# Performance work log

Hardware: AMD Instinct MI355X
Metric: run time of the kernel (lower is better)

The kernel has to match this reference:

```python
import jax, jax.numpy as jnp
import numpy as np

N_NODES = 100000
N_EDGES = 1600000
IN_FEATS = 128
OUT_FEATS = 128
LN_EPS = 1e-5


def setup_inputs() -> dict:
    key = jax.random.key(0)
    k1, k2, k3, k4, k5 = jax.random.split(key, 5)
    h = jax.random.normal(k1, (N_NODES, IN_FEATS), dtype=jnp.float32)
    # nn.Linear(2*in_feats, out_feats): weight [out, 2*in], bias [out]
    stdv = 1.0 / np.sqrt(2 * IN_FEATS)
    W = jax.random.uniform(k2, (OUT_FEATS, 2 * IN_FEATS), dtype=jnp.float32, minval=-stdv, maxval=stdv)
    b = jax.random.uniform(k3, (OUT_FEATS,), dtype=jnp.float32, minval=-stdv, maxval=stdv)
    gamma = jnp.ones((OUT_FEATS,), dtype=jnp.float32)
    beta = jnp.zeros((OUT_FEATS,), dtype=jnp.float32)
    src = jax.random.randint(k4, (N_EDGES,), 0, N_NODES, dtype=jnp.int32)
    dst = jax.random.randint(k5, (N_EDGES,), 0, N_NODES, dtype=jnp.int32)
    return {"h": h, "W": W, "b": b, "gamma": gamma, "beta": beta, "src": src, "dst": dst}


def reference(h, W, b, gamma, beta, src, dst):
    n = h.shape[0]
    ones = jnp.ones(src.shape[0], dtype=h.dtype)
    deg = jax.ops.segment_sum(ones, dst, num_segments=n)          # in-degrees [N]
    norm = jnp.where(deg > 0, 1.0 / deg, 0.0)[:, None]            # inf -> 0
    ah = jax.ops.segment_sum(h[src], dst, num_segments=n)         # copy_src + sum: [N, D]
    cat = jnp.concatenate([h, ah * norm], axis=1)                 # [N, 2D]
    y = cat @ W.T + b                                             # linear -> [N, OUT]
    mu = jnp.mean(y, axis=-1, keepdims=True)
    var = jnp.mean((y - mu) ** 2, axis=-1, keepdims=True)
    y = (y - mu) * jax.lax.rsqrt(var + LN_EPS) * gamma + beta     # LayerNorm
    return jax.nn.relu(y)
```

## Files before the change

### kernel.cpp

```cpp
#include <hip/hip_runtime.h>
#include <hip/hip_bf16.h>

#define LN_EPS 1e-5f

#define NW 4096
#define CHUNK_CAP 96

#define CAP2 1280

typedef __attribute__((ext_vector_type(8))) short short8;
typedef __attribute__((ext_vector_type(4))) float f32x4;
typedef __attribute__((ext_vector_type(2))) float f32x2;
typedef __attribute__((ext_vector_type(4))) int int4v;
typedef __attribute__((ext_vector_type(4))) unsigned int uint4v;

#if defined(__has_builtin)
# if __has_builtin(__builtin_amdgcn_cvt_pk_f32_fp8)
#  define HAS_HW_FP8 1
# endif
#endif
#ifndef HAS_HW_FP8
# define HAS_HW_FP8 0
#endif

__device__ __forceinline__ float b2f(unsigned short u) {
    union { unsigned int i; float f; } x; x.i = ((unsigned int)u) << 16; return x.f;
}
__device__ __forceinline__ unsigned short f2b(float f) {
    unsigned int u = __float_as_uint(f);
    unsigned int r = (u + 0x7FFFu + ((u >> 16) & 1u)) >> 16;
    return (unsigned short)r;
}
__device__ __forceinline__ float loadf(const void* p, long long i, int flag) {
    return flag ? ((const float*)p)[i] : b2f(((const unsigned short*)p)[i]);
}

__device__ __forceinline__ unsigned char f2fp8(float x) {
    float ax = fabsf(x);
    unsigned char s = (unsigned char)((__float_as_uint(x) >> 24) & 0x80);
    if (ax >= 448.f) return s | 0x7E;
    if (ax < 0.015625f) {
        int m = (int)(ax * 512.f + 0.5f);
        return s | (unsigned char)m;
    }
    unsigned u = __float_as_uint(ax);
    int e = (int)((u >> 23) & 0xFF) - 127;
    unsigned m = u & 0x7FFFFF;
    unsigned mr = (m + 0x7FFFF + ((m >> 20) & 1)) >> 20;
    unsigned val = (unsigned)((e + 7) << 3) + mr;
    if (val > 0x7E) val = 0x7E;
    return s | (unsigned char)val;
}
__device__ __forceinline__ float fp8d(unsigned v) {
    unsigned s = (v & 0x80) << 24;
    unsigned e = (v >> 3) & 0xF;
    unsigned m = v & 7;
    if (e == 0) {
        float f = (float)m * 0.001953125f;
        return __uint_as_float(s | __float_as_uint(f));
    }
    return __uint_as_float(s | ((e + 120) << 23) | (m << 20));
}
__device__ __forceinline__ void dec16(uint4 u, float* acc) {
#if HAS_HW_FP8
    f32x2 p;
    p = __builtin_amdgcn_cvt_pk_f32_fp8((int)u.x, false); acc[0] += p[0];  acc[1] += p[1];
    p = __builtin_amdgcn_cvt_pk_f32_fp8((int)u.x, true);  acc[2] += p[0];  acc[3] += p[1];
    p = __builtin_amdgcn_cvt_pk_f32_fp8((int)u.y, false); acc[4] += p[0];  acc[5] += p[1];
    p = __builtin_amdgcn_cvt_pk_f32_fp8((int)u.y, true);  acc[6] += p[0];  acc[7] += p[1];
    p = __builtin_amdgcn_cvt_pk_f32_fp8((int)u.z, false); acc[8] += p[0];  acc[9] += p[1];
    p = __builtin_amdgcn_cvt_pk_f32_fp8((int)u.z, true);  acc[10] += p[0]; acc[11] += p[1];
    p = __builtin_amdgcn_cvt_pk_f32_fp8((int)u.w, false); acc[12] += p[0]; acc[13] += p[1];
    p = __builtin_amdgcn_cvt_pk_f32_fp8((int)u.w, true);  acc[14] += p[0]; acc[15] += p[1];
#else
    acc[0] += fp8d(u.x & 0xFF); acc[1] += fp8d((u.x >> 8) & 0xFF);
    acc[2] += fp8d((u.x >> 16) & 0xFF); acc[3] += fp8d(u.x >> 24);
    acc[4] += fp8d(u.y & 0xFF); acc[5] += fp8d((u.y >> 8) & 0xFF);
    acc[6] += fp8d((u.y >> 16) & 0xFF); acc[7] += fp8d(u.y >> 24);
    acc[8] += fp8d(u.z & 0xFF); acc[9] += fp8d((u.z >> 8) & 0xFF);
    acc[10] += fp8d((u.z >> 16) & 0xFF); acc[11] += fp8d(u.z >> 24);
    acc[12] += fp8d(u.w & 0xFF); acc[13] += fp8d((u.w >> 8) & 0xFF);
    acc[14] += fp8d((u.w >> 16) & 0xFF); acc[15] += fp8d(u.w >> 24);
#endif
}

__global__ __launch_bounds__(256) void prep_cvt_kernel(
    const void* __restrict__ h, unsigned char* __restrict__ h8,
    int* __restrict__ cnt, int* __restrict__ flag, int n_nodes, int n16) {
    __shared__ int sflag;
    const int tid = threadIdx.x;
    if (tid < 64) {
        const unsigned short* hb = (const unsigned short*)h;
        int bad = 0;
        unsigned short u = hb[2 * tid];        int e = (u >> 7) & 0xFF; bad += (e < 96 || e > 135);
        u = hb[2 * (tid + 64)];                e = (u >> 7) & 0xFF;     bad += (e < 96 || e > 135);
#pragma unroll
        for (int off = 1; off < 64; off <<= 1) bad += __shfl_xor(bad, off);
        if (tid == 0) sflag = (bad > 32) ? 1 : 0;
    }
    __syncthreads();
    const int f = sflag;
    const int idx = blockIdx.x * 256 + tid;
    if (idx < n_nodes) cnt[idx] = 0;
    if (idx == 0) *flag = f;
    if (idx < n16) {
        long long base = (long long)idx * 16;
        union { uint4 v; unsigned char b[16]; } o;
        if (f == 0) {
            const unsigned short* hb = (const unsigned short*)h + base;
#pragma unroll
            for (int j = 0; j < 16; ++j) o.b[j] = f2fp8(b2f(hb[j]));
        } else {
            const float* hf = (const float*)h + base;
#pragma unroll
            for (int j = 0; j < 16; ++j) o.b[j] = f2fp8(hf[j]);
        }
        *(uint4*)(h8 + base) = o.v;
    }
}

__global__ __launch_bounds__(256) void bin_kernel(
    const int* __restrict__ src, const int* __restrict__ dst,
    long long* __restrict__ bins,
    int* __restrict__ wcnt,
    int n_edges, int part_nodes) {
    const int g = blockIdx.x * 4 + (threadIdx.x >> 6);
    const int lane = threadIdx.x & 63;
    const int epw = (n_edges + NW - 1) / NW;
    const int e0 = g * epw;
    const int e1 = min(e0 + epw, n_edges);
    const unsigned long long below = (1ull << lane) - 1ull;
    const int t4 = part_nodes * 4, t2 = part_nodes * 2;

    int cur0 = 0, cur1 = 0, cur2 = 0, cur3 = 0, cur4 = 0, cur5 = 0, cur6 = 0, cur7 = 0;

    for (int e = e0 + lane;; e += 64) {
        const bool valid = (e < e1);
        if (!__ballot(valid)) break;
        int d = 0, s = 0;
        if (valid) {
            d = __builtin_nontemporal_load(&dst[e]);
            s = __builtin_nontemporal_load(&src[e]);
        }
        int p = 0, dd = d;
        if (dd >= t4) { p += 4; dd -= t4; }
        if (dd >= t2) { p += 2; dd -= t2; }
        if (dd >= part_nodes) { p += 1; }

        int myoff = CHUNK_CAP;
#pragma unroll
        for (int pp = 0; pp < 8; ++pp) {
            const unsigned long long m = __ballot(valid && (p == pp));
            const int rank = __popcll(m & below);
            const int n = __popcll(m);
            int c = (pp == 0) ? cur0 : (pp == 1) ? cur1 : (pp == 2) ? cur2 :
                    (pp == 3) ? cur3 : (pp == 4) ? cur4 : (pp == 5) ? cur5 :
                    (pp == 6) ? cur6 : cur7;
            if (valid && (p == pp)) myoff = c + rank;
            c += n;
            if (pp == 0) cur0 = c; else if (pp == 1) cur1 = c;
            else if (pp == 2) cur2 = c; else if (pp == 3) cur3 = c;
            else if (pp == 4) cur4 = c; else if (pp == 5) cur5 = c;
            else if (pp == 6) cur6 = c; else cur7 = c;
        }
        if (valid && myoff < CHUNK_CAP) {
            const long long pr = ((long long)(unsigned)d << 32) | (unsigned)s;
            bins[((long long)g * 8 + p) * CHUNK_CAP + myoff] = pr;
        }
    }
    int myc = cur0;
    myc = (lane == 1) ? cur1 : myc;  myc = (lane == 2) ? cur2 : myc;
    myc = (lane == 3) ? cur3 : myc;  myc = (lane == 4) ? cur4 : myc;
    myc = (lane == 5) ? cur5 : myc;  myc = (lane == 6) ? cur6 : myc;
    myc = (lane == 7) ? cur7 : myc;
    if (lane < 8) wcnt[g * 8 + lane] = min(myc, CHUNK_CAP);
}

__global__ __launch_bounds__(256) void regroup_kernel(
    const long long* __restrict__ bins, const int* __restrict__ wcnt,
    long long* __restrict__ bins2, int* __restrict__ gcur,
    int part_nodes) {
    __shared__ int bcnt[256], gbase_s[256], bcur_s[256];
    const int part = blockIdx.x & 7;
    const int rng  = blockIdx.x >> 3;
    const int wbase = rng * 64;
    const int tid = threadIdx.x;
    const int fb_lo = (part * part_nodes) >> 6;
    bcnt[tid] = 0;
    __syncthreads();
    const int wv = tid >> 6, lane = tid & 63;
    for (int c = wv; c < 64; c += 4) {
        const int w = wbase + c;
        const int n = wcnt[w * 8 + part];
        const long long* cb = bins + ((long long)w * 8 + part) * CHUNK_CAP;
        for (int i = lane; i < n; i += 64) {
            const int d = (int)((unsigned long long)cb[i] >> 32);
            atomicAdd(&bcnt[(d >> 6) - fb_lo], 1);
        }
    }
    __syncthreads();
    {
        const int c = bcnt[tid];
        gbase_s[tid] = (c > 0) ? atomicAdd(&gcur[fb_lo + tid], c) : 0;
        bcur_s[tid] = 0;
    }
    __syncthreads();
    for (int c = wv; c < 64; c += 4) {
        const int w = wbase + c;
        const int n = wcnt[w * 8 + part];
        const long long* cb = bins + ((long long)w * 8 + part) * CHUNK_CAP;
        for (int i = lane; i < n; i += 64) {
            const long long pr = cb[i];
            const int d = (int)((unsigned long long)pr >> 32);
            const int lb = (d >> 6) - fb_lo;
            const int r = atomicAdd(&bcur_s[lb], 1);
            const int pos = gbase_s[lb] + r;
            if (pos < CAP2)
                bins2[(long long)(fb_lo + lb) * CAP2 + pos] = pr;
        }
    }
}

__global__ __launch_bounds__(256) void gather_gemm_ln_kernel(
    const unsigned char* __restrict__ h8,
    const long long* __restrict__ bins2,
    const int* __restrict__ gcur,
    const void* __restrict__ h,
    const void* __restrict__ W,
    const void* __restrict__ bias,
    const void* __restrict__ gamma,
    const void* __restrict__ beta,
    void* __restrict__ out,
    const int* __restrict__ flagp,
    int n_nodes) {

    __shared__ __align__(16) unsigned short Atile[64 * 264];
    __shared__ __align__(16) char pool[CAP2 * 4 * 2 + CAP2];
    __shared__ int ncnt[64], noff[64], ncur[64];
    __shared__ unsigned char perm[64];
    __shared__ float2 mrs[64];

    int* sraw = (int*)pool;
    int* slist = sraw + CAP2;
    unsigned char* draw = (unsigned char*)(slist + CAP2);
    float2* pS = (float2*)pool;

    const int flag = *flagp;
    const int tid = threadIdx.x;
    const int fb = blockIdx.x;
    const int nb0 = fb << 6;

    {
        const int seg = tid & 31;
        const int r0 = tid >> 5;
        if (seg < 16) {
            if (flag == 0) {
                const unsigned short* hb = (const unsigned short*)h;
#pragma unroll
                for (int j = 0; j < 8; ++j) {
                    int row = r0 + j * 8;
                    int node = nb0 + row;
                    if (node >= n_nodes) node = n_nodes - 1;
                    short8 val = __builtin_nontemporal_load(
                        (const short8*)(hb + (long long)node * 128 + seg * 8));
                    *(short8*)&Atile[row * 264 + seg * 8] = val;
                }
            } else {
                const float* hfp = (const float*)h;
#pragma unroll
                for (int j = 0; j < 8; ++j) {
                    int row = r0 + j * 8;
                    int node = nb0 + row;
                    if (node >= n_nodes) node = n_nodes - 1;
                    const float* p = hfp + (long long)node * 128 + seg * 8;
                    f32x4 a = __builtin_nontemporal_load((const f32x4*)p);
                    f32x4 b4 = __builtin_nontemporal_load(((const f32x4*)p) + 1);
                    short8 val;
                    val[0] = (short)f2b(a[0]);  val[1] = (short)f2b(a[1]);
                    val[2] = (short)f2b(a[2]);  val[3] = (short)f2b(a[3]);
                    val[4] = (short)f2b(b4[0]); val[5] = (short)f2b(b4[1]);
                    val[6] = (short)f2b(b4[2]); val[7] = (short)f2b(b4[3]);
                    *(short8*)&Atile[row * 264 + seg * 8] = val;
                }
            }
        }
    }

    if (tid < 64) ncnt[tid] = 0;
    __syncthreads();
    const int T = min(gcur[fb], CAP2);
    const long long* bb = bins2 + (long long)fb * CAP2;
    for (int i = tid; i < T; i += 256) {
        const long long pr = __builtin_nontemporal_load(&bb[i]);
        const int ld = ((int)((unsigned long long)pr >> 32)) & 63;
        sraw[i] = (int)(pr & 0xFFFFFFFFll);
        draw[i] = (unsigned char)ld;
        atomicAdd(&ncnt[ld], 1);
    }
    __syncthreads();
    if (tid < 64) {
        const int mydeg = ncnt[tid];
        int o = 0, rk = 0;
#pragma unroll 1
        for (int j = 0; j < 64; ++j) {
            const int dj = ncnt[j];
            o += (j < tid) ? dj : 0;
            rk += (dj > mydeg) || (dj == mydeg && j < tid);
        }
        noff[tid] = o; ncur[tid] = 0;
        perm[rk] = (unsigned char)tid;
    }
    __syncthreads();
    for (int i = tid; i < T; i += 256) {
        const int ld = draw[i];
        const int r = atomicAdd(&ncur[ld], 1);
        slist[noff[ld] + r] = sraw[i];
    }
    __syncthreads();

    const int wv = tid >> 6, lane = tid & 63, g = lane >> 3, li = lane & 7;
#pragma unroll 1
    for (int pass = 0; pass < 2; ++pass) {
        const int rank = (pass * 8 + g) * 4 + wv;
        const int ld = perm[rank];
        const int node = nb0 + ld;
        const bool nvalid = (node < n_nodes);
        const int deg = nvalid ? ncnt[ld] : 0;
        const int ofs = noff[ld];
        int mn = deg, mx = deg;
        mn = min(mn, __shfl_xor(mn, 8));  mx = max(mx, __shfl_xor(mx, 8));
        mn = min(mn, __shfl_xor(mn, 16)); mx = max(mx, __shfl_xor(mx, 16));
        mn = min(mn, __shfl_xor(mn, 32)); mx = max(mx, __shfl_xor(mx, 32));

        float acc[16];
#pragma unroll
        for (int j = 0; j < 16; ++j) acc[j] = 0.f;

        int e = 0;
        for (; e + 1 < mn; e += 2) {
            const int s0 = slist[ofs + e];
            const int s1 = slist[ofs + e + 1];
            uint4 u0 = *(const uint4*)(h8 + (long long)s0 * 128 + li * 16);
            uint4 u1 = *(const uint4*)(h8 + (long long)s1 * 128 + li * 16);
            dec16(u0, acc);
            dec16(u1, acc);
        }
        for (; e < mx; ++e) {
            const bool v = (e < deg);
            const int s = slist[min(ofs + (v ? e : 0), CAP2 - 1)];
            uint4 u = *(const uint4*)(h8 + (long long)(v ? s : 0) * 128 + li * 16);
            if (!v) { u.x = 0u; u.y = 0u; u.z = 0u; u.w = 0u; }
            dec16(u, acc);
        }

        const float nrm = deg > 0 ? 1.f / (float)deg : 0.f;
        short8 a0, a1;
        a0[0] = (short)f2b(acc[0] * nrm);  a0[1] = (short)f2b(acc[1] * nrm);
        a0[2] = (short)f2b(acc[2] * nrm);  a0[3] = (short)f2b(acc[3] * nrm);
        a0[4] = (short)f2b(acc[4] * nrm);  a0[5] = (short)f2b(acc[5] * nrm);
        a0[6] = (short)f2b(acc[6] * nrm);  a0[7] = (short)f2b(acc[7] * nrm);
        a1[0] = (short)f2b(acc[8] * nrm);  a1[1] = (short)f2b(acc[9] * nrm);
        a1[2] = (short)f2b(acc[10] * nrm); a1[3] = (short)f2b(acc[11] * nrm);
        a1[4] = (short)f2b(acc[12] * nrm); a1[5] = (short)f2b(acc[13] * nrm);
        a1[6] = (short)f2b(acc[14] * nrm); a1[7] = (short)f2b(acc[15] * nrm);
        *(short8*)&Atile[ld * 264 + 128 + li * 16] = a0;
        *(short8*)&Atile[ld * 264 + 128 + li * 16 + 8] = a1;
    }
    __syncthreads();

    const int q = lane >> 4;
    const int c = lane & 15;

    short8 bfrag[8][2];
    if (flag == 0) {
        const unsigned short* Wb = (const unsigned short*)W;
#pragma unroll
        for (int ki = 0; ki < 8; ++ki)
#pragma unroll
            for (int t2 = 0; t2 < 2; ++t2)
                bfrag[ki][t2] = *(const short8*)&Wb[(wv * 32 + t2 * 16 + c) * 256 + ki * 32 + q * 8];
    } else {
        const float* Wf = (const float*)W;
#pragma unroll
        for (int ki = 0; ki < 8; ++ki)
#pragma unroll
            for (int t2 = 0; t2 < 2; ++t2) {
                const float* p = Wf + (wv * 32 + t2 * 16 + c) * 256 + ki * 32 + q * 8;
#pragma unroll
                for (int j = 0; j < 8; ++j) bfrag[ki][t2][j] = (short)f2b(p[j]);
            }
    }

    f32x4 acc2[4][2];
#pragma unroll
    for (int rc = 0; rc < 4; ++rc)
#pragma unroll
        for (int t2 = 0; t2 < 2; ++t2) acc2[rc][t2] = (f32x4){0.f, 0.f, 0.f, 0.f};

#pragma unroll
    for (int ki = 0; ki < 8; ++ki) {
        const int kk = ki * 32 + q * 8;
#pragma unroll
        for (int rc = 0; rc < 4; ++rc) {
            const short8 a = *(const short8*)&Atile[(rc * 16 + c) * 264 + kk];
            acc2[rc][0] = __builtin_amdgcn_mfma_f32_16x16x32_bf16(a, bfrag[ki][0], acc2[rc][0], 0, 0, 0);
            acc2[rc][1] = __builtin_amdgcn_mfma_f32_16x16x32_bf16(a, bfrag[ki][1], acc2[rc][1], 0, 0, 0);
        }
    }

    float bcol[2], gcol[2], ecol[2];
#pragma unroll
    for (int t2 = 0; t2 < 2; ++t2) {
        int col = wv * 32 + t2 * 16 + c;
        bcol[t2] = loadf(bias, col, flag);
        gcol[t2] = loadf(gamma, col, flag);
        ecol[t2] = loadf(beta, col, flag);
    }

#pragma unroll
    for (int rc = 0; rc < 4; ++rc)
#pragma unroll
        for (int r = 0; r < 4; ++r) {
            float v0 = acc2[rc][0][r] + bcol[0];
            float v1 = acc2[rc][1][r] + bcol[1];
            float s = v0 + v1;
            float ss = v0 * v0 + v1 * v1;
            s += __shfl_xor(s, 1);  ss += __shfl_xor(ss, 1);
            s += __shfl_xor(s, 2);  ss += __shfl_xor(ss, 2);
            if ((c & 3) == 0) {
                int row = rc * 16 + q * 4 + r;
                pS[row * 17 + (wv * 4 + (c >> 2))] = make_float2(s, ss);
            }
        }
    __syncthreads();

    if (tid < 64) {
        float s = 0.f, ss = 0.f;
#pragma unroll
        for (int j = 0; j < 16; ++j) {
            float2 p = pS[tid * 17 + j];
            s += p.x; ss += p.y;
        }
        float mean = s * (1.f / 128.f);
        float var = ss * (1.f / 128.f) - mean * mean;
        mrs[tid] = make_float2(mean, rsqrtf(var + LN_EPS));
    }
    __syncthreads();

#pragma unroll
    for (int rc = 0; rc < 4; ++rc)
#pragma unroll
        for (int r = 0; r < 4; ++r) {
            int row = rc * 16 + q * 4 + r;
            int node = nb0 + row;
            if (node < n_nodes) {
                float2 m = mrs[row];
#pragma unroll
                for (int t2 = 0; t2 < 2; ++t2) {
                    float o = (acc2[rc][t2][r] + bcol[t2] - m.x) * m.y * gcol[t2] + ecol[t2];
                    o = o > 0.f ? o : 0.f;
                    long long idx = (long long)node * 128 + wv * 32 + t2 * 16 + c;
                    if (flag) ((float*)out)[idx] = o;
                    else      ((unsigned short*)out)[idx] = f2b(o);
                }
            }
        }
}

extern "C" void kernel_launch(void* const* d_in, const int* in_sizes, int n_in,
                              void* d_out, int out_size, void* d_ws, size_t ws_size,
                              hipStream_t stream) {
    const void* h     = d_in[0];
    const void* W     = d_in[1];
    const void* b     = d_in[2];
    const void* gamma = d_in[3];
    const void* beta  = d_in[4];
    const int* src = (const int*)d_in[5];
    const int* dst = (const int*)d_in[6];

    const int n_nodes = in_sizes[0] / 128;
    const int n_edges = in_sizes[5];
    const int part_nodes = (n_nodes + 7) / 8;
    const int nbuckets = (n_nodes + 63) >> 6;

    unsigned short* reg0 = (unsigned short*)d_ws;
    long long* bins2 = (long long*)(reg0 + (size_t)n_nodes * 128);
    int* gcur   = (int*)(bins2) + (size_t)n_nodes * 64;
    int* flag   = gcur + n_nodes;
    unsigned char* h8 = (unsigned char*)(flag + 64);

    long long* bins = (long long*)reg0;
    int* wcnt = (int*)((char*)reg0 + (size_t)NW * 8 * CHUNK_CAP * 8);

    int n16 = n_nodes * 8;
    int pgrid = (max(n16, n_nodes) + 255) / 256;
    prep_cvt_kernel<<<pgrid, 256, 0, stream>>>(h, h8, gcur, flag, n_nodes, n16);

    bin_kernel<<<NW / 4, 256, 0, stream>>>(src, dst, bins, wcnt, n_edges, part_nodes);

    regroup_kernel<<<512, 256, 0, stream>>>(bins, wcnt, bins2, gcur, part_nodes);

    gather_gemm_ln_kernel<<<nbuckets, 256, 0, stream>>>(h8, bins2, gcur, h, W, b,
                                                        gamma, beta, d_out, flag, n_nodes);
}
```

Measured before the change: 275.6 us.

## Pack edge pairs into 32-bit words, use hardware FP8 encode, unroll gather by four

Edge (dst,src) pairs are packed into one 32-bit word (local dst offset in high bits, 17-bit src) instead of 64-bit pairs. This halves bin and bin2 traffic and removes the shared-memory staging copy in the gather kernel, which now re-reads the packed words. The prep conversion uses vector loads and the hardware fp8 pack instruction, and the neighbor gather loop issues four row loads per iteration for more memory-level parallelism. The LayerNorm partial reduction is also done with more shuffles to shrink shared writes. The 17-bit src field limits node count to 131072 and the local dst field to what fits in 15 bits.

```diff
diff --git a/kernel.cpp b/kernel.cpp
--- a/kernel.cpp
+++ b/kernel.cpp
@@ -7,6 +7,8 @@
 #define CHUNK_CAP 96
 
 #define CAP2 1280
+
+#define S_MASK 0x1FFFFu
 
 typedef __attribute__((ext_vector_type(8))) short short8;
 typedef __attribute__((ext_vector_type(4))) float f32x4;
@@ -18,9 +20,15 @@
 # if __has_builtin(__builtin_amdgcn_cvt_pk_f32_fp8)
 #  define HAS_HW_FP8 1
 # endif
+# if __has_builtin(__builtin_amdgcn_cvt_pk_fp8_f32)
+#  define HAS_HW_FP8E 1
+# endif
 #endif
 #ifndef HAS_HW_FP8
 # define HAS_HW_FP8 0
+#endif
+#ifndef HAS_HW_FP8E
+# define HAS_HW_FP8E 0
 #endif
 
 __device__ __forceinline__ float b2f(unsigned short u) {
@@ -50,6 +58,16 @@
     unsigned val = (unsigned)((e + 7) << 3) + mr;
     if (val > 0x7E) val = 0x7E;
     return s | (unsigned char)val;
+}
+__device__ __forceinline__ unsigned enc4(float a, float b, float c, float d) {
+#if HAS_HW_FP8E
+    int r = __builtin_amdgcn_cvt_pk_fp8_f32(a, b, 0, false);
+    r = __builtin_amdgcn_cvt_pk_fp8_f32(c, d, r, true);
+    return (unsigned)r;
+#else
+    return (unsigned)f2fp8(a) | ((unsigned)f2fp8(b) << 8) |
+           ((unsigned)f2fp8(c) << 16) | ((unsigned)f2fp8(d) << 24);
+#endif
 }
 __device__ __forceinline__ float fp8d(unsigned v) {
     unsigned s = (v & 0x80) << 24;
@@ -105,23 +123,37 @@
     if (idx == 0) *flag = f;
     if (idx < n16) {
         long long base = (long long)idx * 16;
-        union { uint4 v; unsigned char b[16]; } o;
+        uint4 o;
         if (f == 0) {
-            const unsigned short* hb = (const unsigned short*)h + base;
-#pragma unroll
-            for (int j = 0; j < 16; ++j) o.b[j] = f2fp8(b2f(hb[j]));
+            const unsigned short* hp = (const unsigned short*)h + base;
+            short8 v0 = *(const short8*)hp;
+            short8 v1 = *(const short8*)(hp + 8);
+            o.x = enc4(b2f((unsigned short)v0[0]), b2f((unsigned short)v0[1]),
+                       b2f((unsigned short)v0[2]), b2f((unsigned short)v0[3]));
+            o.y = enc4(b2f((unsigned short)v0[4]), b2f((unsigned short)v0[5]),
+                       b2f((unsigned short)v0[6]), b2f((unsigned short)v0[7]));
+            o.z = enc4(b2f((unsigned short)v1[0]), b2f((unsigned short)v1[1]),
+                       b2f((unsigned short)v1[2]), b2f((unsigned short)v1[3]));
+            o.w = enc4(b2f((unsigned short)v1[4]), b2f((unsigned short)v1[5]),
+                       b2f((unsigned short)v1[6]), b2f((unsigned short)v1[7]));
         } else {
             const float* hf = (const float*)h + base;
-#pragma unroll
-            for (int j = 0; j < 16; ++j) o.b[j] = f2fp8(hf[j]);
-        }
-        *(uint4*)(h8 + base) = o.v;
+            f32x4 a = *(const f32x4*)hf;
+            f32x4 b4 = *(const f32x4*)(hf + 4);
+            f32x4 c4 = *(const f32x4*)(hf + 8);
+            f32x4 d4 = *(const f32x4*)(hf + 12);
+            o.x = enc4(a[0], a[1], a[2], a[3]);
+            o.y = enc4(b4[0], b4[1], b4[2], b4[3]);
+            o.z = enc4(c4[0], c4[1], c4[2], c4[3]);
+            o.w = enc4(d4[0], d4[1], d4[2], d4[3]);
+        }
+        *(uint4*)(h8 + base) = o;
     }
 }
 
 __global__ __launch_bounds__(256) void bin_kernel(
     const int* __restrict__ src, const int* __restrict__ dst,
-    long long* __restrict__ bins,
+    unsigned* __restrict__ bins,
     int* __restrict__ wcnt,
     int n_edges, int part_nodes) {
     const int g = blockIdx.x * 4 + (threadIdx.x >> 6);
@@ -145,7 +177,7 @@
         int p = 0, dd = d;
         if (dd >= t4) { p += 4; dd -= t4; }
         if (dd >= t2) { p += 2; dd -= t2; }
-        if (dd >= part_nodes) { p += 1; }
+        if (dd >= part_nodes) { p += 1; dd -= part_nodes; }
 
         int myoff = CHUNK_CAP;
 #pragma unroll
@@ -164,7 +196,7 @@
             else if (pp == 6) cur6 = c; else cur7 = c;
         }
         if (valid && myoff < CHUNK_CAP) {
-            const long long pr = ((long long)(unsigned)d << 32) | (unsigned)s;
+            const unsigned pr = ((unsigned)dd << 17) | (unsigned)s;
             bins[((long long)g * 8 + p) * CHUNK_CAP + myoff] = pr;
         }
     }
@@ -177,25 +209,26 @@
 }
 
 __global__ __launch_bounds__(256) void regroup_kernel(
-    const long long* __restrict__ bins, const int* __restrict__ wcnt,
-    long long* __restrict__ bins2, int* __restrict__ gcur,
+    const unsigned* __restrict__ bins, const int* __restrict__ wcnt,
+    unsigned* __restrict__ bins2, int* __restrict__ gcur,
     int part_nodes) {
     __shared__ int bcnt[256], gbase_s[256], bcur_s[256];
     const int part = blockIdx.x & 7;
     const int rng  = blockIdx.x >> 3;
     const int wbase = rng * 64;
     const int tid = threadIdx.x;
-    const int fb_lo = (part * part_nodes) >> 6;
+    const int lo = part * part_nodes;
+    const int fb_lo = lo >> 6;
     bcnt[tid] = 0;
     __syncthreads();
     const int wv = tid >> 6, lane = tid & 63;
     for (int c = wv; c < 64; c += 4) {
         const int w = wbase + c;
         const int n = wcnt[w * 8 + part];
-        const long long* cb = bins + ((long long)w * 8 + part) * CHUNK_CAP;
+        const unsigned* cb = bins + ((long long)w * 8 + part) * CHUNK_CAP;
         for (int i = lane; i < n; i += 64) {
-            const int d = (int)((unsigned long long)cb[i] >> 32);
-            atomicAdd(&bcnt[(d >> 6) - fb_lo], 1);
+            const int node = lo + (int)(cb[i] >> 17);
+            atomicAdd(&bcnt[(node >> 6) - fb_lo], 1);
         }
     }
     __syncthreads();
@@ -208,22 +241,23 @@
     for (int c = wv; c < 64; c += 4) {
         const int w = wbase + c;
         const int n = wcnt[w * 8 + part];
-        const long long* cb = bins + ((long long)w * 8 + part) * CHUNK_CAP;
+        const unsigned* cb = bins + ((long long)w * 8 + part) * CHUNK_CAP;
         for (int i = lane; i < n; i += 64) {
-            const long long pr = cb[i];
-            const int d = (int)((unsigned long long)pr >> 32);
-            const int lb = (d >> 6) - fb_lo;
+            const unsigned pr = cb[i];
+            const int node = lo + (int)(pr >> 17);
+            const int lb = (node >> 6) - fb_lo;
             const int r = atomicAdd(&bcur_s[lb], 1);
             const int pos = gbase_s[lb] + r;
             if (pos < CAP2)
-                bins2[(long long)(fb_lo + lb) * CAP2 + pos] = pr;
+                bins2[(long long)(fb_lo + lb) * CAP2 + pos] =
+                    ((unsigned)(node & 63) << 17) | (pr & S_MASK);
         }
     }
 }
 
 __global__ __launch_bounds__(256) void gather_gemm_ln_kernel(
     const unsigned char* __restrict__ h8,
-    const long long* __restrict__ bins2,
+    const unsigned* __restrict__ bins2,
     const int* __restrict__ gcur,
     const void* __restrict__ h,
     const void* __restrict__ W,
@@ -235,14 +269,12 @@
     int n_nodes) {
 
     __shared__ __align__(16) unsigned short Atile[64 * 264];
-    __shared__ __align__(16) char pool[CAP2 * 4 * 2 + CAP2];
+    __shared__ __align__(16) char pool[CAP2 * 4];
     __shared__ int ncnt[64], noff[64], ncur[64];
     __shared__ unsigned char perm[64];
     __shared__ float2 mrs[64];
 
-    int* sraw = (int*)pool;
-    int* slist = sraw + CAP2;
-    unsigned char* draw = (unsigned char*)(slist + CAP2);
+    int* slist = (int*)pool;
     float2* pS = (float2*)pool;
 
     const int flag = *flagp;
@@ -289,12 +321,9 @@
     if (tid < 64) ncnt[tid] = 0;
     __syncthreads();
     const int T = min(gcur[fb], CAP2);
-    const long long* bb = bins2 + (long long)fb * CAP2;
+    const unsigned* bb = bins2 + (long long)fb * CAP2;
     for (int i = tid; i < T; i += 256) {
-        const long long pr = __builtin_nontemporal_load(&bb[i]);
-        const int ld = ((int)((unsigned long long)pr >> 32)) & 63;
-        sraw[i] = (int)(pr & 0xFFFFFFFFll);
-        draw[i] = (unsigned char)ld;
+        const int ld = (int)(bb[i] >> 17);
         atomicAdd(&ncnt[ld], 1);
     }
     __syncthreads();
@@ -312,9 +341,10 @@
     }
     __syncthreads();
     for (int i = tid; i < T; i += 256) {
-        const int ld = draw[i];
+        const unsigned pr = bb[i];
+        const int ld = (int)(pr >> 17);
         const int r = atomicAdd(&ncur[ld], 1);
-        slist[noff[ld] + r] = sraw[i];
+        slist[noff[ld] + r] = (int)(pr & S_MASK);
     }
     __syncthreads();
 
@@ -337,13 +367,19 @@
         for (int j = 0; j < 16; ++j) acc[j] = 0.f;
 
         int e = 0;
-        for (; e + 1 < mn; e += 2) {
+        for (; e + 3 < mn; e += 4) {
             const int s0 = slist[ofs + e];
             const int s1 = slist[ofs + e + 1];
+            const int s2 = slist[ofs + e + 2];
+            const int s3 = slist[ofs + e + 3];
             uint4 u0 = *(const uint4*)(h8 + (long long)s0 * 128 + li * 16);
             uint4 u1 = *(const uint4*)(h8 + (long long)s1 * 128 + li * 16);
+            uint4 u2 = *(const uint4*)(h8 + (long long)s2 * 128 + li * 16);
+            uint4 u3 = *(const uint4*)(h8 + (long long)s3 * 128 + li * 16);
             dec16(u0, acc);
             dec16(u1, acc);
+            dec16(u2, acc);
+            dec16(u3, acc);
         }
         for (; e < mx; ++e) {
             const bool v = (e < deg);
@@ -427,9 +463,11 @@
             float ss = v0 * v0 + v1 * v1;
             s += __shfl_xor(s, 1);  ss += __shfl_xor(ss, 1);
             s += __shfl_xor(s, 2);  ss += __shfl_xor(ss, 2);
-            if ((c & 3) == 0) {
+            s += __shfl_xor(s, 4);  ss += __shfl_xor(ss, 4);
+            s += __shfl_xor(s, 8);  ss += __shfl_xor(ss, 8);
+            if (c == 0) {
                 int row = rc * 16 + q * 4 + r;
-                pS[row * 17 + (wv * 4 + (c >> 2))] = make_float2(s, ss);
+                pS[row * 5 + wv] = make_float2(s, ss);
             }
         }
     __syncthreads();
@@ -437,8 +475,8 @@
     if (tid < 64) {
         float s = 0.f, ss = 0.f;
 #pragma unroll
-        for (int j = 0; j < 16; ++j) {
-            float2 p = pS[tid * 17 + j];
+        for (int j = 0; j < 4; ++j) {
+            float2 p = pS[tid * 5 + j];
             s += p.x; ss += p.y;
         }
         float mean = s * (1.f / 128.f);
@@ -484,13 +522,13 @@
     const int nbuckets = (n_nodes + 63) >> 6;
 
     unsigned short* reg0 = (unsigned short*)d_ws;
-    long long* bins2 = (long long*)(reg0 + (size_t)n_nodes * 128);
-    int* gcur   = (int*)(bins2) + (size_t)n_nodes * 64;
+    unsigned* bins2 = (unsigned*)(reg0 + (size_t)n_nodes * 128);
+    int* gcur   = (int*)bins2 + (size_t)n_nodes * 64;
     int* flag   = gcur + n_nodes;
     unsigned char* h8 = (unsigned char*)(flag + 64);
 
-    long long* bins = (long long*)reg0;
-    int* wcnt = (int*)((char*)reg0 + (size_t)NW * 8 * CHUNK_CAP * 8);
+    unsigned* bins = (unsigned*)reg0;
+    int* wcnt = (int*)((char*)reg0 + (size_t)NW * 8 * CHUNK_CAP * 4);
 
     int n16 = n_nodes * 8;
     int pgrid = (max(n16, n_nodes) + 255) / 256;
```

After: 243.2 us. -11.7%, faster.
